# Kernel optimization log

Measured on AMD Instinct MI355X. Metric: run time of the kernel, lower is better.

## Reference

```python
import jax, jax.numpy as jnp
import numpy as np

PI = np.pi
B = 1048576   # rays
S = 4         # spheres
H = 2048      # texture height
W = 2048      # texture width
C = 4         # ray_features per sphere
HID = 32
OUT = 3
EPS = 1e-5


def lerp(a, b, t):
    return a + t * (b - a)


def nan_to_num(a):
    return jnp.where(jnp.isfinite(a), a, jnp.zeros_like(a))


def grid_sample(image, x, y):
    """Bilinear gather: image (H, W, C); x, y in [0, 1], shape (B,)."""
    h, w, _ = image.shape
    x = x * (w - 1)
    y = y * (h - 1)
    x0 = jnp.floor(x).astype(jnp.int32)
    x1 = jnp.ceil(x).astype(jnp.int32)
    xf = (x - x0)[:, None]
    y0 = jnp.floor(y).astype(jnp.int32)
    y1 = jnp.ceil(y).astype(jnp.int32)
    yf = (y - y0)[:, None]
    top = lerp(image[y0, x0], image[y0, x1], xf)
    bot = lerp(image[y1, x0], image[y1, x1], xf)
    return lerp(top, bot, yf)


def layernorm(x, g, b):
    m = jnp.mean(x, axis=-1, keepdims=True)
    v = jnp.mean((x - m) ** 2, axis=-1, keepdims=True)
    return (x - m) * jax.lax.rsqrt(v + EPS) * g + b


def setup_inputs() -> dict:
    key = jax.random.key(0)
    ks = jax.random.split(key, 8)
    inputs = jax.random.uniform(ks[0], (B, 2 * S), dtype=jnp.float32) * PI
    sphere_features = jax.random.uniform(ks[1], (S, H, W, C), dtype=jnp.float32)
    d_in = S * C
    w_in = jax.random.normal(ks[2], (d_in, HID), dtype=jnp.float32) * 0.1
    b_in = jnp.zeros((HID,), dtype=jnp.float32)
    g_in = jnp.ones((HID,), dtype=jnp.float32)
    bt_in = jnp.zeros((HID,), dtype=jnp.float32)
    n_hid = 2  # layers - 2
    w_hid = jax.random.normal(ks[3], (n_hid, HID, HID), dtype=jnp.float32) * 0.1
    b_hid = jnp.zeros((n_hid, HID), dtype=jnp.float32)
    g_hid = jnp.ones((n_hid, HID), dtype=jnp.float32)
    bt_hid = jnp.zeros((n_hid, HID), dtype=jnp.float32)
    w_out = jax.random.normal(ks[4], (HID, OUT), dtype=jnp.float32) * 0.1
    b_out = jnp.zeros((OUT,), dtype=jnp.float32)
    return {"inputs": inputs, "sphere_features": sphere_features,
            "w_in": w_in, "b_in": b_in, "g_in": g_in, "bt_in": bt_in,
            "w_hid": w_hid, "b_hid": b_hid, "g_hid": g_hid, "bt_hid": bt_hid,
            "w_out": w_out, "b_out": b_out}


def reference(inputs, sphere_features, w_in, b_in, g_in, bt_in,
              w_hid, b_hid, g_hid, bt_hid, w_out, b_out):
    b = inputs.shape[0]
    theta = inputs[:, 0::2] / (2 * PI)   # (B, S)
    phi = inputs[:, 1::2] / PI           # (B, S)
    finite = jnp.isfinite(theta) & jnp.isfinite(phi)  # (B, S)
    t = nan_to_num(theta)
    p = nan_to_num(phi)
    # vmap over spheres -> (B, S, C)
    feats = jax.vmap(grid_sample, in_axes=(0, 1, 1), out_axes=1)(sphere_features, t, p)
    feats = jnp.where(finite[..., None], feats, jnp.zeros_like(feats))
    x = feats.reshape(b, -1)  # (B, S*C)
    x = jax.nn.relu(layernorm(x @ w_in + b_in, g_in, bt_in))
    for i in range(w_hid.shape[0]):
        x = jax.nn.relu(layernorm(x @ w_hid[i] + b_hid[i], g_hid[i], bt_hid[i]))
    return x @ w_out + b_out
```

## Files before the change

### kernel.cpp

```cpp
#include <hip/hip_runtime.h>
#include <hip/hip_fp16.h>
#include <math.h>
#include <stdint.h>

#define NRAYS   1048576
#define NSPH    4
#define TEXH    2048
#define TEXW    2048
#define DIN     16
#define HID     32
#define NOUT    3
#define LN_EPS  1e-5f

#define CX      325.79013f
#define CY      651.58025f

#define QROWS   2048
#define QW      1024
#define Q_BYTES ((size_t)NSPH * QROWS * QW * 16)

#define WF_OFF   Q_BYTES
#define BI_OFF   (WF_OFF + 7*64*16)
#define LP_OFF   (BI_OFF + (size_t)4*64*32)
#define WS_NEEDED (LP_OFF + (size_t)3*64*64)

#define SB() __builtin_amdgcn_sched_barrier(0)

typedef _Float16 half8  __attribute__((ext_vector_type(8)));
typedef _Float16 half2v __attribute__((ext_vector_type(2)));
typedef float    floatx4 __attribute__((ext_vector_type(4)));

__device__ __forceinline__ int pkh(float a, float b) {
    return __builtin_bit_cast(int, __builtin_amdgcn_cvt_pkrtz(a, b));
}

__device__ __forceinline__ uint32_t pack8(const float4 v) {
    const uint32_t r = (uint32_t)(v.x * 255.0f + 0.5f);
    const uint32_t g = (uint32_t)(v.y * 255.0f + 0.5f);
    const uint32_t b = (uint32_t)(v.z * 255.0f + 0.5f);
    const uint32_t a = (uint32_t)(v.w * 255.0f + 0.5f);
    return r | (g << 8) | (b << 16) | (a << 24);
}

__global__ __launch_bounds__(256) void relayout_kernel(
    const float* __restrict__ tex, uint4* __restrict__ Q)
{
    const int x = blockIdx.x * 256 + threadIdx.x;
    const int y = blockIdx.y;
    const int s = blockIdx.z;
    const int y1 = min(y + 1, TEXH - 1);
    const float4* img = reinterpret_cast<const float4*>(tex) + (size_t)s * TEXH * TEXW;
    const float4 t00 = img[(size_t)y  * TEXW + x];
    const float4 t01 = img[(size_t)y  * TEXW + x + 1];
    const float4 t10 = img[(size_t)y1 * TEXW + x];
    const float4 t11 = img[(size_t)y1 * TEXW + x + 1];
    uint4 q;
    q.x = pack8(t00); q.y = pack8(t01); q.z = pack8(t10); q.w = pack8(t11);
    Q[((size_t)s * QROWS + y) * QW + x] = q;
}

__global__ __launch_bounds__(64) void prep_w(
    const float* __restrict__ w_in,  const float* __restrict__ b_in,
    const float* __restrict__ g_in,  const float* __restrict__ bt_in,
    const float* __restrict__ w_hid, const float* __restrict__ b_hid,
    const float* __restrict__ g_hid, const float* __restrict__ bt_hid,
    const float* __restrict__ w_out, const float* __restrict__ b_out,
    char* __restrict__ wsb)
{
    const int l  = threadIdx.x;
    const int m  = l & 15;
    const int kg = l >> 4;
    int4* WF = (int4*)(wsb + WF_OFF);

    #pragma unroll
    for (int f = 0; f < 2; ++f) {
        half8 v;
        #pragma unroll
        for (int j = 0; j < 8; ++j) {
            const int k = kg * 8 + j;
            v[j] = (_Float16)((k < DIN) ? w_in[k * HID + f * 16 + m] : 0.0f);
        }
        WF[f * 64 + l] = __builtin_bit_cast(int4, v);
    }
    #pragma unroll
    for (int t = 0; t < 2; ++t)
        #pragma unroll
        for (int hf = 0; hf < 2; ++hf) {
            half8 v;
            #pragma unroll
            for (int j = 0; j < 8; ++j) {
                const int k = kg * 8 + j;
                v[j] = (_Float16)w_hid[t * HID * HID + k * HID + hf * 16 + m];
            }
            WF[(2 + t * 2 + hf) * 64 + l] = __builtin_bit_cast(int4, v);
        }
    {
        half8 v;
        #pragma unroll
        for (int j = 0; j < 8; ++j) {
            const int k = kg * 8 + j;
            v[j] = (_Float16)((m < NOUT) ? w_out[k * NOUT + m] : 0.0f);
        }
        WF[6 * 64 + l] = __builtin_bit_cast(int4, v);
    }

    floatx4* BI = (floatx4*)(wsb + BI_OFF);
    const int r0 = kg * 4;
    floatx4 lo, hi;
    #pragma unroll
    for (int i = 0; i < 4; ++i) { lo[i] = b_in[r0 + i]; hi[i] = b_in[16 + r0 + i]; }
    BI[(0 * 64 + l) * 2 + 0] = lo; BI[(0 * 64 + l) * 2 + 1] = hi;
    #pragma unroll
    for (int i = 0; i < 4; ++i) { lo[i] = b_hid[r0 + i]; hi[i] = b_hid[16 + r0 + i]; }
    BI[(1 * 64 + l) * 2 + 0] = lo; BI[(1 * 64 + l) * 2 + 1] = hi;
    #pragma unroll
    for (int i = 0; i < 4; ++i) { lo[i] = b_hid[32 + r0 + i]; hi[i] = b_hid[48 + r0 + i]; }
    BI[(2 * 64 + l) * 2 + 0] = lo; BI[(2 * 64 + l) * 2 + 1] = hi;
    #pragma unroll
    for (int i = 0; i < 4; ++i) { lo[i] = (r0 + i < NOUT) ? b_out[r0 + i] : 0.0f; hi[i] = 0.0f; }
    BI[(3 * 64 + l) * 2 + 0] = lo; BI[(3 * 64 + l) * 2 + 1] = hi;

    floatx4* LP = (floatx4*)(wsb + LP_OFF);
    floatx4 a, b, c, d;
    #pragma unroll
    for (int i = 0; i < 4; ++i) {
        a[i] = g_in[r0 + i];  b[i] = g_in[16 + r0 + i];
        c[i] = bt_in[r0 + i]; d[i] = bt_in[16 + r0 + i];
    }
    LP[(0 * 64 + l) * 4 + 0] = a; LP[(0 * 64 + l) * 4 + 1] = b;
    LP[(0 * 64 + l) * 4 + 2] = c; LP[(0 * 64 + l) * 4 + 3] = d;
    #pragma unroll
    for (int t = 0; t < 2; ++t) {
        #pragma unroll
        for (int i = 0; i < 4; ++i) {
            a[i] = g_hid[t * 32 + r0 + i];  b[i] = g_hid[t * 32 + 16 + r0 + i];
            c[i] = bt_hid[t * 32 + r0 + i]; d[i] = bt_hid[t * 32 + 16 + r0 + i];
        }
        LP[((1 + t) * 64 + l) * 4 + 0] = a; LP[((1 + t) * 64 + l) * 4 + 1] = b;
        LP[((1 + t) * 64 + l) * 4 + 2] = c; LP[((1 + t) * 64 + l) * 4 + 3] = d;
    }
}

__device__ __forceinline__ half8 ln_b(int t, floatx4 a0, floatx4 a1,
                                      int lane, const floatx4* __restrict__ LP) {
    float s = 0.0f, q = 0.0f;
    #pragma unroll
    for (int i = 0; i < 4; ++i) {
        s += a0[i] + a1[i];
        q = fmaf(a0[i], a0[i], q);
        q = fmaf(a1[i], a1[i], q);
    }
    s += __shfl_xor(s, 16);
    s += __shfl_xor(s, 32);
    q += __shfl_xor(q, 16);
    q += __shfl_xor(q, 32);
    const float m   = s * (1.0f / 32.0f);
    const float var = fmaf(q, 1.0f / 32.0f, -m * m);
    const float r   = rsqrtf(var + LN_EPS);
    const floatx4 g0 = LP[(t * 64 + lane) * 4 + 0];
    const floatx4 g1 = LP[(t * 64 + lane) * 4 + 1];
    const floatx4 b0 = LP[(t * 64 + lane) * 4 + 2];
    const floatx4 b1 = LP[(t * 64 + lane) * 4 + 3];
    float h0[4], h1[4];
    #pragma unroll
    for (int i = 0; i < 4; ++i) {
        h0[i] = fmaxf(0.0f, fmaf((a0[i] - m) * r, g0[i], b0[i]));
        h1[i] = fmaxf(0.0f, fmaf((a1[i] - m) * r, g1[i], b1[i]));
    }
    const int ph0 = pkh(h0[0], h0[1]), ph1 = pkh(h0[2], h0[3]);
    const int ph2 = pkh(h1[0], h1[1]), ph3 = pkh(h1[2], h1[3]);
    const int c = lane & 15, G = lane >> 4;
    const int slo = ((G & 1) * 32 + c) * 4;
    int bdw[4];
    #pragma unroll
    for (int d = 0; d < 4; ++d) {
        const int sl  = slo + (d >> 1) * 64;
        const int plo = (d & 1) ? ph1 : ph0;
        const int phi = (d & 1) ? ph3 : ph2;
        const int rlo = __builtin_amdgcn_ds_bpermute(sl, plo);
        const int rhi = __builtin_amdgcn_ds_bpermute(sl, phi);
        bdw[d] = (G < 2) ? rlo : rhi;
    }
    const int4 bi = make_int4(bdw[0], bdw[1], bdw[2], bdw[3]);
    return __builtin_bit_cast(half8, bi);
}

__device__ __forceinline__ float ubv(uint32_t w, int c) {
    return (float)((w >> (8 * c)) & 0xFFu);
}

__global__ __launch_bounds__(256, 3) void ray_mlp_mfma(
    const float* __restrict__ inputs,
    const uint4* __restrict__ Q,
    const char* __restrict__ wsb,
    float* __restrict__ out)
{
    const int lane = threadIdx.x & 63;
    const int ray  = blockIdx.x * 256 + threadIdx.x;
    const int ray_base = ray - lane;

    const float4 in0 = *reinterpret_cast<const float4*>(inputs + (size_t)ray * 8);
    const float4 in1 = *reinterpret_cast<const float4*>(inputs + (size_t)ray * 8 + 4);
    const float th[NSPH] = {in0.x, in0.z, in1.x, in1.z};
    const float ph[NSPH] = {in0.y, in0.w, in1.y, in1.w};

    float xf[NSPH], yf[NSPH], fm[NSPH];
    uint32_t off[NSPH];
    #pragma unroll
    for (int s = 0; s < NSPH; ++s) {
        float fx = th[s] * CX;
        float fy = ph[s] * CY;
        const bool fin = isfinite(fx) && isfinite(fy);
        fm[s] = fin ? (1.0f / 255.0f) : 0.0f;
        fx = fin ? fx : 0.0f;
        fy = fin ? fy : 0.0f;
        const float fx0 = floorf(fx), fy0 = floorf(fy);
        xf[s] = fx - fx0;
        yf[s] = fy - fy0;
        const uint32_t x0 = (uint32_t)min(max((int)fx0, 0), QW - 1);
        const uint32_t y0 = (uint32_t)min(max((int)fy0, 0), QROWS - 1);
        off[s] = ((((uint32_t)s << 11) + y0) << 10) + x0;
    }
    uint4 q[NSPH];
    #pragma unroll
    for (int s = 0; s < NSPH; ++s) q[s] = Q[off[s]];
    SB();

    float x[DIN];
    #pragma unroll
    for (int s = 0; s < NSPH; ++s) {
        const float xfs = xf[s], yfs = yf[s], m = fm[s];
        #pragma unroll
        for (int c = 0; c < 4; ++c) {
            const float f00 = ubv(q[s].x, c);
            const float f01 = ubv(q[s].y, c);
            const float f10 = ubv(q[s].z, c);
            const float f11 = ubv(q[s].w, c);
            const float top = fmaf(xfs, f01 - f00, f00);
            const float bot = fmaf(xfs, f11 - f10, f10);
            x[4 * s + c] = fmaf(yfs, bot - top, top) * m;
        }
    }

    int xh[8];
    #pragma unroll
    for (int j = 0; j < 8; ++j) xh[j] = pkh(x[2 * j], x[2 * j + 1]);

    const int4* WF = (const int4*)(wsb + WF_OFF);
    int4 af[7];
    #pragma unroll
    for (int f = 0; f < 7; ++f) af[f] = WF[f * 64 + lane];

    const floatx4* BI = (const floatx4*)(wsb + BI_OFF);
    const floatx4* LP = (const floatx4*)(wsb + LP_OFF);

    const int c = lane & 15, G = lane >> 4;

    #pragma unroll 1
    for (int g = 0; g < 4; ++g) {
        const int srcb = (g * 16 + c) * 4;
        int bdw[4];
        #pragma unroll
        for (int d = 0; d < 4; ++d) {
            const int r0 = __builtin_amdgcn_ds_bpermute(srcb, xh[d]);
            const int r1 = __builtin_amdgcn_ds_bpermute(srcb, xh[4 + d]);
            bdw[d] = (G == 0) ? r0 : (G == 1) ? r1 : 0;
        }
        half8 B = __builtin_bit_cast(half8, make_int4(bdw[0], bdw[1], bdw[2], bdw[3]));

        floatx4 acc0 = BI[(0 * 64 + lane) * 2 + 0];
        floatx4 acc1 = BI[(0 * 64 + lane) * 2 + 1];
        acc0 = __builtin_amdgcn_mfma_f32_16x16x32_f16(__builtin_bit_cast(half8, af[0]), B, acc0, 0, 0, 0);
        acc1 = __builtin_amdgcn_mfma_f32_16x16x32_f16(__builtin_bit_cast(half8, af[1]), B, acc1, 0, 0, 0);
        B = ln_b(0, acc0, acc1, lane, LP);

        acc0 = BI[(1 * 64 + lane) * 2 + 0];
        acc1 = BI[(1 * 64 + lane) * 2 + 1];
        acc0 = __builtin_amdgcn_mfma_f32_16x16x32_f16(__builtin_bit_cast(half8, af[2]), B, acc0, 0, 0, 0);
        acc1 = __builtin_amdgcn_mfma_f32_16x16x32_f16(__builtin_bit_cast(half8, af[3]), B, acc1, 0, 0, 0);
        B = ln_b(1, acc0, acc1, lane, LP);

        acc0 = BI[(2 * 64 + lane) * 2 + 0];
        acc1 = BI[(2 * 64 + lane) * 2 + 1];
        acc0 = __builtin_amdgcn_mfma_f32_16x16x32_f16(__builtin_bit_cast(half8, af[4]), B, acc0, 0, 0, 0);
        acc1 = __builtin_amdgcn_mfma_f32_16x16x32_f16(__builtin_bit_cast(half8, af[5]), B, acc1, 0, 0, 0);
        B = ln_b(2, acc0, acc1, lane, LP);

        floatx4 acco = BI[(3 * 64 + lane) * 2 + 0];
        acco = __builtin_amdgcn_mfma_f32_16x16x32_f16(__builtin_bit_cast(half8, af[6]), B, acco, 0, 0, 0);

        if (lane < 16) {
            const size_t ro = (size_t)(ray_base + g * 16 + lane) * 3;
            out[ro + 0] = acco[0];
            out[ro + 1] = acco[1];
            out[ro + 2] = acco[2];
        }
    }
}

__device__ __forceinline__ void ln_relu_apply(float* __restrict__ pre,
                                              const float* __restrict__ g,
                                              const float* __restrict__ bt,
                                              float* __restrict__ h) {
    float m = 0.0f;
    #pragma unroll
    for (int j = 0; j < HID; ++j) m += pre[j];
    m *= (1.0f / HID);
    float v = 0.0f;
    #pragma unroll
    for (int j = 0; j < HID; ++j) { pre[j] -= m; v = fmaf(pre[j], pre[j], v); }
    const float r = rsqrtf(fmaf(v, (1.0f / HID), LN_EPS));
    #pragma unroll
    for (int j = 0; j < HID; ++j)
        h[j] = fmaxf(0.0f, fmaf(pre[j] * r, g[j], bt[j]));
}

__global__ __launch_bounds__(256, 4) void ray_mlp_direct(
    const float* __restrict__ inputs, const float* __restrict__ tex,
    const float* __restrict__ w_in,  const float* __restrict__ b_in,
    const float* __restrict__ g_in,  const float* __restrict__ bt_in,
    const float* __restrict__ w_hid, const float* __restrict__ b_hid,
    const float* __restrict__ g_hid, const float* __restrict__ bt_hid,
    const float* __restrict__ w_out, const float* __restrict__ b_out,
    float* __restrict__ out) {
    const int ray = blockIdx.x * 256 + threadIdx.x;
    const float4 in0 = *reinterpret_cast<const float4*>(inputs + (size_t)ray * 8);
    const float4 in1 = *reinterpret_cast<const float4*>(inputs + (size_t)ray * 8 + 4);
    const float th[NSPH] = {in0.x, in0.z, in1.x, in1.z};
    const float ph[NSPH] = {in0.y, in0.w, in1.y, in1.w};
    float x[DIN];
    #pragma unroll
    for (int s = 0; s < NSPH; ++s) {
        float fx = th[s] * CX, fy = ph[s] * CY;
        const bool fin = isfinite(fx) && isfinite(fy);
        const float fmv = fin ? 1.0f : 0.0f;
        fx = fin ? fx : 0.0f; fy = fin ? fy : 0.0f;
        const float fx0 = floorf(fx), fy0 = floorf(fy);
        const float xf = fx - fx0, yf = fy - fy0;
        const int x0 = min(max((int)fx0, 0), TEXW - 1);
        const int x1 = min(max((int)ceilf(fx), 0), TEXW - 1);
        const int y0 = min(max((int)fy0, 0), TEXH - 1);
        const int y1 = min(max((int)ceilf(fy), 0), TEXH - 1);
        const float4* img = reinterpret_cast<const float4*>(tex) + (size_t)s * TEXH * TEXW;
        const float4 t00 = img[(size_t)y0 * TEXW + x0];
        const float4 t01 = img[(size_t)y0 * TEXW + x1];
        const float4 t10 = img[(size_t)y1 * TEXW + x0];
        const float4 t11 = img[(size_t)y1 * TEXW + x1];
        float tp0 = fmaf(xf, t01.x - t00.x, t00.x), tp1 = fmaf(xf, t01.y - t00.y, t00.y);
        float tp2 = fmaf(xf, t01.z - t00.z, t00.z), tp3 = fmaf(xf, t01.w - t00.w, t00.w);
        float bt0 = fmaf(xf, t11.x - t10.x, t10.x), bt1 = fmaf(xf, t11.y - t10.y, t10.y);
        float bt2 = fmaf(xf, t11.z - t10.z, t10.z), bt3 = fmaf(xf, t11.w - t10.w, t10.w);
        x[4*s+0] = fmaf(yf, bt0 - tp0, tp0) * fmv;
        x[4*s+1] = fmaf(yf, bt1 - tp1, tp1) * fmv;
        x[4*s+2] = fmaf(yf, bt2 - tp2, tp2) * fmv;
        x[4*s+3] = fmaf(yf, bt3 - tp3, tp3) * fmv;
    }
    float pre[HID], h[HID];
    #pragma unroll
    for (int j = 0; j < HID; ++j) pre[j] = b_in[j];
    #pragma unroll
    for (int k = 0; k < DIN; ++k) {
        const float xv = x[k];
        #pragma unroll
        for (int j = 0; j < HID; ++j)
            pre[j] = fmaf(xv, w_in[k * HID + j], pre[j]);
    }
    ln_relu_apply(pre, g_in, bt_in, h);
    #pragma unroll
    for (int l = 0; l < 2; ++l) {
        const float* __restrict__ W  = w_hid  + l * HID * HID;
        const float* __restrict__ bb = b_hid  + l * HID;
        const float* __restrict__ gg = g_hid  + l * HID;
        const float* __restrict__ bt = bt_hid + l * HID;
        #pragma unroll
        for (int j = 0; j < HID; ++j) pre[j] = bb[j];
        #pragma unroll
        for (int k = 0; k < HID; ++k) {
            const float hv = h[k];
            #pragma unroll
            for (int j = 0; j < HID; ++j)
                pre[j] = fmaf(hv, W[k * HID + j], pre[j]);
        }
        ln_relu_apply(pre, gg, bt, h);
    }
    float o0 = b_out[0], o1 = b_out[1], o2 = b_out[2];
    #pragma unroll
    for (int k = 0; k < HID; ++k) {
        const float hv = h[k];
        o0 = fmaf(hv, w_out[k * NOUT + 0], o0);
        o1 = fmaf(hv, w_out[k * NOUT + 1], o1);
        o2 = fmaf(hv, w_out[k * NOUT + 2], o2);
    }
    out[(size_t)ray * NOUT + 0] = o0;
    out[(size_t)ray * NOUT + 1] = o1;
    out[(size_t)ray * NOUT + 2] = o2;
}

extern "C" void kernel_launch(void* const* d_in, const int* in_sizes, int n_in,
                              void* d_out, int out_size, void* d_ws, size_t ws_size,
                              hipStream_t stream) {
    const float* inputs = (const float*)d_in[0];
    const float* tex    = (const float*)d_in[1];
    const float* w_in   = (const float*)d_in[2];
    const float* b_in   = (const float*)d_in[3];
    const float* g_in   = (const float*)d_in[4];
    const float* bt_in  = (const float*)d_in[5];
    const float* w_hid  = (const float*)d_in[6];
    const float* b_hid  = (const float*)d_in[7];
    const float* g_hid  = (const float*)d_in[8];
    const float* bt_hid = (const float*)d_in[9];
    const float* w_out  = (const float*)d_in[10];
    const float* b_out  = (const float*)d_in[11];
    float* out = (float*)d_out;

    if (ws_size >= WS_NEEDED) {
        char* wsb = (char*)d_ws;
        uint4* Q = (uint4*)wsb;
        relayout_kernel<<<dim3(QW / 256, QROWS, NSPH), 256, 0, stream>>>(tex, Q);
        prep_w<<<1, 64, 0, stream>>>(w_in, b_in, g_in, bt_in,
                                     w_hid, b_hid, g_hid, bt_hid,
                                     w_out, b_out, wsb);
        ray_mlp_mfma<<<NRAYS / 256, 256, 0, stream>>>(inputs, Q, wsb, out);
    } else {
        ray_mlp_direct<<<NRAYS / 256, 256, 0, stream>>>(
            inputs, tex, w_in, b_in, g_in, bt_in,
            w_hid, b_hid, g_hid, bt_hid, w_out, b_out, out);
    }
}
```

Baseline: 155.4 us.

## Gather textures directly into MFMA B-fragment layout and interleave two MLP chains

Each lane now gathers texture features for two rays and two spheres, arranged so the packed fp16 values already sit in the MFMA B-operand layout. This replaces the per-group ds_bpermute shuffles with one xor-32 shuffle. The MLP loop is fully unrolled into two phases, each running two independent 16-ray chains so their MFMAs and layernorms can interleave. Bias and weight fragment loads are hoisted out of the loop and issued earlier. The cost is higher register pressure under the launch bound of 3 blocks per SM, which may cause spills or lower occupancy.

```diff
diff --git a/kernel.cpp b/kernel.cpp
--- a/kernel.cpp
+++ b/kernel.cpp
@@ -27,7 +27,6 @@
 #define SB() __builtin_amdgcn_sched_barrier(0)
 
 typedef _Float16 half8  __attribute__((ext_vector_type(8)));
-typedef _Float16 half2v __attribute__((ext_vector_type(2)));
 typedef float    floatx4 __attribute__((ext_vector_type(4)));
 
 __device__ __forceinline__ int pkh(float a, float b) {
@@ -196,104 +195,153 @@
     float* __restrict__ out)
 {
     const int lane = threadIdx.x & 63;
-    const int ray  = blockIdx.x * 256 + threadIdx.x;
-    const int ray_base = ray - lane;
-
-    const float4 in0 = *reinterpret_cast<const float4*>(inputs + (size_t)ray * 8);
-    const float4 in1 = *reinterpret_cast<const float4*>(inputs + (size_t)ray * 8 + 4);
-    const float th[NSPH] = {in0.x, in0.z, in1.x, in1.z};
-    const float ph[NSPH] = {in0.y, in0.w, in1.y, in1.w};
-
-    float xf[NSPH], yf[NSPH], fm[NSPH];
-    uint32_t off[NSPH];
-    #pragma unroll
-    for (int s = 0; s < NSPH; ++s) {
-        float fx = th[s] * CX;
-        float fy = ph[s] * CY;
+    const int wv   = threadIdx.x >> 6;
+    const int ray_base = blockIdx.x * 256 + wv * 64;
+
+    const int c = lane & 15;
+    const int u = (lane >> 4) & 1;
+    const int p = lane >> 5;
+
+    const int rA = ray_base + p * 32 + c;
+    const int rB = rA + 16;
+
+    const float4 angA = *reinterpret_cast<const float4*>(inputs + (size_t)rA * 8 + 4 * u);
+    const float4 angB = *reinterpret_cast<const float4*>(inputs + (size_t)rB * 8 + 4 * u);
+
+    const int s0 = 2 * u;
+
+    float xf[4], yf[4], fm[4];
+    uint32_t off[4];
+    const float thv[4] = {angA.x, angA.z, angB.x, angB.z};
+    const float phv[4] = {angA.y, angA.w, angB.y, angB.w};
+    #pragma unroll
+    for (int i = 0; i < 4; ++i) {
+        const int s = s0 + (i & 1);
+        float fx = thv[i] * CX;
+        float fy = phv[i] * CY;
         const bool fin = isfinite(fx) && isfinite(fy);
-        fm[s] = fin ? (1.0f / 255.0f) : 0.0f;
+        fm[i] = fin ? (1.0f / 255.0f) : 0.0f;
         fx = fin ? fx : 0.0f;
         fy = fin ? fy : 0.0f;
         const float fx0 = floorf(fx), fy0 = floorf(fy);
-        xf[s] = fx - fx0;
-        yf[s] = fy - fy0;
+        xf[i] = fx - fx0;
+        yf[i] = fy - fy0;
         const uint32_t x0 = (uint32_t)min(max((int)fx0, 0), QW - 1);
         const uint32_t y0 = (uint32_t)min(max((int)fy0, 0), QROWS - 1);
-        off[s] = ((((uint32_t)s << 11) + y0) << 10) + x0;
-    }
-    uint4 q[NSPH];
-    #pragma unroll
-    for (int s = 0; s < NSPH; ++s) q[s] = Q[off[s]];
+        off[i] = ((((uint32_t)s << 11) + y0) << 10) + x0;
+    }
+
+    uint4 q0 = Q[off[0]];
+    uint4 q1 = Q[off[1]];
+    uint4 q2 = Q[off[2]];
+    uint4 q3 = Q[off[3]];
+    const int4* WF = (const int4*)(wsb + WF_OFF);
+    int4 af0 = WF[0 * 64 + lane], af1 = WF[1 * 64 + lane];
+    int4 af2 = WF[2 * 64 + lane], af3 = WF[3 * 64 + lane];
+    int4 af4 = WF[4 * 64 + lane], af5 = WF[5 * 64 + lane];
+    int4 af6 = WF[6 * 64 + lane];
     SB();
 
-    float x[DIN];
-    #pragma unroll
-    for (int s = 0; s < NSPH; ++s) {
-        const float xfs = xf[s], yfs = yf[s], m = fm[s];
-        #pragma unroll
-        for (int c = 0; c < 4; ++c) {
-            const float f00 = ubv(q[s].x, c);
-            const float f01 = ubv(q[s].y, c);
-            const float f10 = ubv(q[s].z, c);
-            const float f11 = ubv(q[s].w, c);
-            const float top = fmaf(xfs, f01 - f00, f00);
-            const float bot = fmaf(xfs, f11 - f10, f10);
-            x[4 * s + c] = fmaf(yfs, bot - top, top) * m;
-        }
-    }
-
-    int xh[8];
-    #pragma unroll
-    for (int j = 0; j < 8; ++j) xh[j] = pkh(x[2 * j], x[2 * j + 1]);
-
-    const int4* WF = (const int4*)(wsb + WF_OFF);
-    int4 af[7];
-    #pragma unroll
-    for (int f = 0; f < 7; ++f) af[f] = WF[f * 64 + lane];
+    float fA[8], fB[8];
+    {
+        const uint4 qq[4] = {q0, q1, q2, q3};
+        #pragma unroll
+        for (int i = 0; i < 4; ++i) {
+            const float xfs = xf[i], yfs = yf[i], m = fm[i];
+            float* dst = (i < 2) ? fA : fB;
+            const int base = (i & 1) * 4;
+            #pragma unroll
+            for (int ch = 0; ch < 4; ++ch) {
+                const float f00 = ubv(qq[i].x, ch);
+                const float f01 = ubv(qq[i].y, ch);
+                const float f10 = ubv(qq[i].z, ch);
+                const float f11 = ubv(qq[i].w, ch);
+                const float top = fmaf(xfs, f01 - f00, f00);
+                const float bot = fmaf(xfs, f11 - f10, f10);
+                dst[base + ch] = fmaf(yfs, bot - top, top) * m;
+            }
+        }
+    }
+    const int dA0 = pkh(fA[0], fA[1]), dA1 = pkh(fA[2], fA[3]);
+    const int dA2 = pkh(fA[4], fA[5]), dA3 = pkh(fA[6], fA[7]);
+    const int dB0 = pkh(fB[0], fB[1]), dB1 = pkh(fB[2], fB[3]);
+    const int dB2 = pkh(fB[4], fB[5]), dB3 = pkh(fB[6], fB[7]);
 
     const floatx4* BI = (const floatx4*)(wsb + BI_OFF);
     const floatx4* LP = (const floatx4*)(wsb + LP_OFF);
 
-    const int c = lane & 15, G = lane >> 4;
-
-    #pragma unroll 1
-    for (int g = 0; g < 4; ++g) {
-        const int srcb = (g * 16 + c) * 4;
-        int bdw[4];
-        #pragma unroll
-        for (int d = 0; d < 4; ++d) {
-            const int r0 = __builtin_amdgcn_ds_bpermute(srcb, xh[d]);
-            const int r1 = __builtin_amdgcn_ds_bpermute(srcb, xh[4 + d]);
-            bdw[d] = (G == 0) ? r0 : (G == 1) ? r1 : 0;
-        }
-        half8 B = __builtin_bit_cast(half8, make_int4(bdw[0], bdw[1], bdw[2], bdw[3]));
-
-        floatx4 acc0 = BI[(0 * 64 + lane) * 2 + 0];
-        floatx4 acc1 = BI[(0 * 64 + lane) * 2 + 1];
-        acc0 = __builtin_amdgcn_mfma_f32_16x16x32_f16(__builtin_bit_cast(half8, af[0]), B, acc0, 0, 0, 0);
-        acc1 = __builtin_amdgcn_mfma_f32_16x16x32_f16(__builtin_bit_cast(half8, af[1]), B, acc1, 0, 0, 0);
-        B = ln_b(0, acc0, acc1, lane, LP);
-
-        acc0 = BI[(1 * 64 + lane) * 2 + 0];
-        acc1 = BI[(1 * 64 + lane) * 2 + 1];
-        acc0 = __builtin_amdgcn_mfma_f32_16x16x32_f16(__builtin_bit_cast(half8, af[2]), B, acc0, 0, 0, 0);
-        acc1 = __builtin_amdgcn_mfma_f32_16x16x32_f16(__builtin_bit_cast(half8, af[3]), B, acc1, 0, 0, 0);
-        B = ln_b(1, acc0, acc1, lane, LP);
-
-        acc0 = BI[(2 * 64 + lane) * 2 + 0];
-        acc1 = BI[(2 * 64 + lane) * 2 + 1];
-        acc0 = __builtin_amdgcn_mfma_f32_16x16x32_f16(__builtin_bit_cast(half8, af[4]), B, acc0, 0, 0, 0);
-        acc1 = __builtin_amdgcn_mfma_f32_16x16x32_f16(__builtin_bit_cast(half8, af[5]), B, acc1, 0, 0, 0);
-        B = ln_b(2, acc0, acc1, lane, LP);
-
-        floatx4 acco = BI[(3 * 64 + lane) * 2 + 0];
-        acco = __builtin_amdgcn_mfma_f32_16x16x32_f16(__builtin_bit_cast(half8, af[6]), B, acco, 0, 0, 0);
+    const floatx4 bi00 = BI[(0 * 64 + lane) * 2 + 0];
+    const floatx4 bi01 = BI[(0 * 64 + lane) * 2 + 1];
+    const floatx4 bi10 = BI[(1 * 64 + lane) * 2 + 0];
+    const floatx4 bi11 = BI[(1 * 64 + lane) * 2 + 1];
+    const floatx4 bi20 = BI[(2 * 64 + lane) * 2 + 0];
+    const floatx4 bi21 = BI[(2 * 64 + lane) * 2 + 1];
+    const floatx4 bi30 = BI[(3 * 64 + lane) * 2 + 0];
+
+    const half8 haf0 = __builtin_bit_cast(half8, af0);
+    const half8 haf1 = __builtin_bit_cast(half8, af1);
+    const half8 haf2 = __builtin_bit_cast(half8, af2);
+    const half8 haf3 = __builtin_bit_cast(half8, af3);
+    const half8 haf4 = __builtin_bit_cast(half8, af4);
+    const half8 haf5 = __builtin_bit_cast(half8, af5);
+    const half8 haf6 = __builtin_bit_cast(half8, af6);
+
+    #pragma unroll
+    for (int ph = 0; ph < 2; ++ph) {
+        int e0, e1, e2, e3, f0, f1, f2, f3;
+        if (ph == 0) {
+            const bool sel = (p == 0);
+            e0 = sel ? dA0 : 0; e1 = sel ? dA1 : 0; e2 = sel ? dA2 : 0; e3 = sel ? dA3 : 0;
+            f0 = sel ? dB0 : 0; f1 = sel ? dB1 : 0; f2 = sel ? dB2 : 0; f3 = sel ? dB3 : 0;
+        } else {
+            const bool sel = (lane < 32);
+            const int sA0 = __shfl_xor(dA0, 32), sA1 = __shfl_xor(dA1, 32);
+            const int sA2 = __shfl_xor(dA2, 32), sA3 = __shfl_xor(dA3, 32);
+            const int sB0 = __shfl_xor(dB0, 32), sB1 = __shfl_xor(dB1, 32);
+            const int sB2 = __shfl_xor(dB2, 32), sB3 = __shfl_xor(dB3, 32);
+            e0 = sel ? sA0 : 0; e1 = sel ? sA1 : 0; e2 = sel ? sA2 : 0; e3 = sel ? sA3 : 0;
+            f0 = sel ? sB0 : 0; f1 = sel ? sB1 : 0; f2 = sel ? sB2 : 0; f3 = sel ? sB3 : 0;
+        }
+        half8 B0 = __builtin_bit_cast(half8, make_int4(e0, e1, e2, e3));
+        half8 B1 = __builtin_bit_cast(half8, make_int4(f0, f1, f2, f3));
+
+        floatx4 a00 = bi00, a01 = bi01, a10 = bi00, a11 = bi01;
+        a00 = __builtin_amdgcn_mfma_f32_16x16x32_f16(haf0, B0, a00, 0, 0, 0);
+        a10 = __builtin_amdgcn_mfma_f32_16x16x32_f16(haf0, B1, a10, 0, 0, 0);
+        a01 = __builtin_amdgcn_mfma_f32_16x16x32_f16(haf1, B0, a01, 0, 0, 0);
+        a11 = __builtin_amdgcn_mfma_f32_16x16x32_f16(haf1, B1, a11, 0, 0, 0);
+        B0 = ln_b(0, a00, a01, lane, LP);
+        B1 = ln_b(0, a10, a11, lane, LP);
+
+        a00 = bi10; a01 = bi11; a10 = bi10; a11 = bi11;
+        a00 = __builtin_amdgcn_mfma_f32_16x16x32_f16(haf2, B0, a00, 0, 0, 0);
+        a10 = __builtin_amdgcn_mfma_f32_16x16x32_f16(haf2, B1, a10, 0, 0, 0);
+        a01 = __builtin_amdgcn_mfma_f32_16x16x32_f16(haf3, B0, a01, 0, 0, 0);
+        a11 = __builtin_amdgcn_mfma_f32_16x16x32_f16(haf3, B1, a11, 0, 0, 0);
+        B0 = ln_b(1, a00, a01, lane, LP);
+        B1 = ln_b(1, a10, a11, lane, LP);
+
+        a00 = bi20; a01 = bi21; a10 = bi20; a11 = bi21;
+        a00 = __builtin_amdgcn_mfma_f32_16x16x32_f16(haf4, B0, a00, 0, 0, 0);
+        a10 = __builtin_amdgcn_mfma_f32_16x16x32_f16(haf4, B1, a10, 0, 0, 0);
+        a01 = __builtin_amdgcn_mfma_f32_16x16x32_f16(haf5, B0, a01, 0, 0, 0);
+        a11 = __builtin_amdgcn_mfma_f32_16x16x32_f16(haf5, B1, a11, 0, 0, 0);
+        B0 = ln_b(2, a00, a01, lane, LP);
+        B1 = ln_b(2, a10, a11, lane, LP);
+
+        floatx4 o0 = bi30, o1 = bi30;
+        o0 = __builtin_amdgcn_mfma_f32_16x16x32_f16(haf6, B0, o0, 0, 0, 0);
+        o1 = __builtin_amdgcn_mfma_f32_16x16x32_f16(haf6, B1, o1, 0, 0, 0);
 
         if (lane < 16) {
-            const size_t ro = (size_t)(ray_base + g * 16 + lane) * 3;
-            out[ro + 0] = acco[0];
-            out[ro + 1] = acco[1];
-            out[ro + 2] = acco[2];
+            const size_t r0 = (size_t)(ray_base + (2 * ph) * 16 + lane) * 3;
+            out[r0 + 0] = o0[0];
+            out[r0 + 1] = o0[1];
+            out[r0 + 2] = o0[2];
+            const size_t r1 = (size_t)(ray_base + (2 * ph + 1) * 16 + lane) * 3;
+            out[r1 + 0] = o1[0];
+            out[r1 + 1] = o1[1];
+            out[r1 + 2] = o1[2];
         }
     }
 }
```

Result: no change. 157.0 us (+1.0%).
